# Kernel optimization log

Measured on AMD Instinct MI355X. Metric: run time of the kernel, lower is better.

## Reference

```python
import jax, jax.numpy as jnp
import numpy as np

NUM_CLASSES = 8
UP = 3


def _espcn_params(key):
    k1, k2, k3 = jax.random.split(key, 3)
    # conv1: 5x5, 1->64 ; conv2: 3x3, 64->32 ; conv3: 3x3, 32->UP^2
    w1 = jax.random.normal(k1, (64, 1, 5, 5), jnp.float32) * 0.05
    b1 = jnp.zeros((64,), jnp.float32)
    w2 = jax.random.normal(k2, (32, 64, 3, 3), jnp.float32) * 0.05
    b2 = jnp.zeros((32,), jnp.float32)
    w3 = jax.random.normal(k3, (UP * UP, 32, 3, 3), jnp.float32) * 0.05
    b3 = jnp.zeros((UP * UP,), jnp.float32)
    return (w1, b1, w2, b2, w3, b3)


def setup_inputs() -> dict:
    key = jax.random.key(0)
    kx, kc, kp = jax.random.split(key, 3)
    x = jax.random.uniform(kx, (32, 1, 128, 128), jnp.float32)
    class_indices = jax.random.randint(kc, (32,), 0, NUM_CLASSES, jnp.int32)
    # Stack per-expert params along leading expert axis
    keys = jax.random.split(kp, NUM_CLASSES)
    per = [_espcn_params(k) for k in keys]
    stacked = [jnp.stack([p[i] for p in per], axis=0) for i in range(6)]
    w1, b1, w2, b2, w3, b3 = stacked
    return {"x": x, "class_indices": class_indices,
            "w1": w1, "b1": b1, "w2": w2, "b2": b2, "w3": w3, "b3": b3}


def _conv(x, w, b, pad):
    y = jax.lax.conv_general_dilated(
        x, w, window_strides=(1, 1), padding=[(pad, pad), (pad, pad)],
        dimension_numbers=("NCHW", "OIHW", "NCHW"))
    return y + b[None, :, None, None]


def _pixel_shuffle(x, r):
    b, c, h, w = x.shape
    oc = c // (r * r)
    x = x.reshape(b, oc, r, r, h, w)
    x = x.transpose(0, 1, 4, 2, 5, 3)  # b, oc, h, r, w, r
    return x.reshape(b, oc, h * r, w * r)


def _espcn(x, w1, b1, w2, b2, w3, b3):
    h = jnp.tanh(_conv(x, w1, b1, 2))
    h = jnp.tanh(_conv(h, w2, b2, 1))
    h = _conv(h, w3, b3, 1)
    return _pixel_shuffle(h, UP)


def reference(x, class_indices, w1, b1, w2, b2, w3, b3):
    # Run every expert on the full batch (faithful to original dense dispatch),
    # then mask-and-sum via one-hot routing weights.
    one_hot = jax.nn.one_hot(class_indices, NUM_CLASSES, dtype=x.dtype)  # [B, E]

    def run_expert(params):
        ew1, eb1, ew2, eb2, ew3, eb3 = params
        return _espcn(x, ew1, eb1, ew2, eb2, ew3, eb3)  # [B, C, H*r, W*r]

    outs = jax.vmap(run_expert)((w1, b1, w2, b2, w3, b3))  # [E, B, C, H', W']
    weights = one_hot.T[:, :, None, None, None]  # [E, B, 1, 1, 1]
    return jnp.sum(outs * weights, axis=0)
```

## Files before the change

kernel.cpp:

```cpp
#include <hip/hip_runtime.h>

#define NE 8
#define HW 128
#define OUT_HW 384
#define C1 64
#define C2 32
#define C3 9

typedef __attribute__((ext_vector_type(4))) float f32x4;
typedef __attribute__((ext_vector_type(8))) short bf16x8s;
typedef __attribute__((ext_vector_type(2))) unsigned u32x2;

__device__ __align__(16) unsigned short g_w1b[NE * C1 * 32];
__device__ __align__(16) unsigned short g_w2b[NE * 9 * C2 * C1];
__device__ __align__(16) unsigned short g_w3b[NE * 9 * 16 * 32];

__device__ __forceinline__ unsigned short f2bf(float f) {
    unsigned u = __builtin_bit_cast(unsigned, f);
    u += 0x7fffu + ((u >> 16) & 1u);
    return (unsigned short)(u >> 16);
}

__device__ __forceinline__ unsigned cvt_pk_bf16(float lo, float hi) {
    unsigned r;
    asm("v_cvt_pk_bf16_f32 %0, %1, %2" : "=v"(r) : "v"(lo), "v"(hi));
    return r;
}

__global__ void repack_weights_kernel(const float* __restrict__ w1,
                                      const float* __restrict__ w2,
                                      const float* __restrict__ w3) {
    int i = blockIdx.x * 256 + threadIdx.x;
    const int n2 = NE * C2 * C1 * 9;
    const int n1 = NE * C1 * 32;
    const int n3 = NE * 9 * 16 * 32;
    if (i < n2) {
        int e = i / (C2 * C1 * 9);
        int r = i - e * (C2 * C1 * 9);
        int oc = r / (C1 * 9); r -= oc * (C1 * 9);
        int ic = r / 9;
        int koff = r - ic * 9;
        g_w2b[((e * 9 + koff) * C2 + oc) * C1 + ic] = f2bf(w2[i]);
    } else if (i < n2 + n1) {
        int j = i - n2;
        int tap = j & 31;
        int eoc = j >> 5;
        float v = (tap < 25) ? w1[eoc * 25 + tap] : 0.f;
        g_w1b[j] = f2bf(v);
    } else if (i < n2 + n1 + n3) {
        int j = i - n2 - n1;
        int e = j / (9 * 16 * 32);
        int r = j - e * (9 * 16 * 32);
        int koff = r / 512; r -= koff * 512;
        int oc = r / 32;
        int ic = r - oc * 32;
        float v = 0.f;
        if (oc < C3) v = w3[((e * C3 + oc) * 32 + ic) * 9 + koff];
        g_w3b[((e * 9 + koff) * 16 + oc) * 32 + ic] = f2bf(v);
    }
}

__device__ __forceinline__ float fast_tanh(float x) {
    float u = __builtin_amdgcn_exp2f(x * 2.88539008f);
    return 1.0f - 2.0f * __builtin_amdgcn_rcpf(1.0f + u);
}

__launch_bounds__(512, 4)
__global__ void espcn_fused_kernel(const float* __restrict__ x,
                                   const int* __restrict__ ci,
                                   const float* __restrict__ b1,
                                   const float* __restrict__ b2,
                                   const float* __restrict__ b3,
                                   float* __restrict__ out) {
    __shared__ __align__(16) char ldsp[79200];
    float (*xs)[25]   = (float(*)[25])ldsp;
    char* imc         = ldsp + 2400;
    char* h2b         = ldsp + 2400;
    char* h1s         = ldsp + 28000;
    float (*outT)[52] = (float(*)[52])(ldsp + 28000);

    const int tx = blockIdx.x, ty = blockIdx.y, b = blockIdx.z;
    const int R0 = ty * 16, C0 = tx * 16;
    const bool interior = (tx >= 1) && (tx <= 6) && (ty >= 1) && (ty <= 6);
    int e = ci[b];
    e = __builtin_amdgcn_readfirstlane(e);
    const int t = threadIdx.x;
    const int lane = t & 63, wave = t >> 6;
    const int g = lane >> 4, r16 = lane & 15;

    #pragma unroll
    for (int it = 0; it < 2; ++it) {
        int idx = it * 512 + t;
        if (idx < 576) {
            int ii = idx / 24, jj = idx - ii * 24;
            int gy = R0 - 4 + ii, gx = C0 - 4 + jj;
            float v = 0.f;
            if (interior || ((unsigned)gy < (unsigned)HW && (unsigned)gx < (unsigned)HW))
                v = x[(b * HW + gy) * HW + gx];
            xs[ii][jj] = v;
        }
    }
    __syncthreads();

    {
        const int w = t & 15, pr = t >> 4;
        int t0 = 2 * w;     if (t0 > 24) t0 = 24;
        int t1 = 2 * w + 1; if (t1 > 24) t1 = 24;
        const int dy0 = t0 / 5, dx0 = t0 - 5 * (t0 / 5);
        const int dy1 = t1 / 5, dx1 = t1 - 5 * (t1 / 5);
        const bool v0 = (2 * w) < 25, v1 = (2 * w + 1) < 25;
        const int swz = (w * 4) ^ ((pr & 3) << 4);
        #pragma unroll
        for (int it = 0; it < 13; ++it) {
            int p = it * 32 + pr;
            if (p < 400) {
                int i = p / 20, j = p - i * 20;
                float f0 = v0 ? xs[i + dy0][j + dx0] : 0.f;
                float f1 = v1 ? xs[i + dy1][j + dx1] : 0.f;
                *(unsigned*)(imc + p * 64 + swz) = cvt_pk_bf16(f0, f1);
            }
        }
    }
    __syncthreads();

    {
        const unsigned short* w1e = g_w1b + e * C1 * 32;
        const int octile = wave & 3, hi = wave >> 2;
        bf16x8s W = *(const bf16x8s*)(w1e + (octile * 16 + r16) * 32 + g * 8);
        f32x4 bias4 = *(const f32x4*)(b1 + e * C1 + octile * 16 + g * 4);
        const int imcb = r16 * 64 + ((g * 16) ^ ((r16 & 3) << 4));
        const int h1b = (r16 << 7) + ((octile * 32 + g * 8) ^ ((r16 & 7) << 4));
        #pragma unroll
        for (int k = 0; k < 13; ++k) {
            int pt = hi + 2 * k;
            if (pt < 25) {
                bf16x8s I = *(const bf16x8s*)(imc + pt * 1024 + imcb);
                f32x4 acc = {0.f, 0.f, 0.f, 0.f};
                acc = __builtin_amdgcn_mfma_f32_16x16x32_bf16(W, I, acc, 0, 0, 0);
                float s0 = fast_tanh(acc[0] + bias4[0]);
                float s1 = fast_tanh(acc[1] + bias4[1]);
                float s2 = fast_tanh(acc[2] + bias4[2]);
                float s3 = fast_tanh(acc[3] + bias4[3]);
                if (!interior) {
                    int p = pt * 16 + r16;
                    int i = p / 20, j = p - i * 20;
                    int gy = R0 - 2 + i, gx = C0 - 2 + j;
                    bool in = ((unsigned)gy < (unsigned)HW) && ((unsigned)gx < (unsigned)HW);
                    if (!in) { s0 = 0.f; s1 = 0.f; s2 = 0.f; s3 = 0.f; }
                }
                u32x2 hv = { cvt_pk_bf16(s0, s1), cvt_pk_bf16(s2, s3) };
                *(u32x2*)(h1s + h1b + pt * 2048) = hv;
            }
        }
    }
    __syncthreads();

    {
        const unsigned short* w2e = g_w2b + e * 9 * C2 * C1;
        const bool has2 = (wave + 16) < 21;
        const int pt0 = wave, pt1 = wave + 8, pt2 = has2 ? wave + 16 : wave;
        int ab[3];
        {
            int pts[3] = {pt0, pt1, pt2};
            #pragma unroll
            for (int s3 = 0; s3 < 3; ++s3) {
                int px = pts[s3] * 16 + r16; if (px > 323) px = 323;
                int r = px / 18, c = px - r * 18;
                ab[s3] = r * 20 + c;
            }
        }
        int rb[3][9];
        #pragma unroll
        for (int s3 = 0; s3 < 3; ++s3)
            #pragma unroll
            for (int k = 0; k < 9; ++k) {
                int ap = ab[s3] + (k / 3) * 20 + (k % 3);
                rb[s3][k] = (ap << 7) | ((ap & 7) << 4);
            }
        f32x4 a00 = {0.f,0.f,0.f,0.f}, a01 = {0.f,0.f,0.f,0.f};
        f32x4 a10 = {0.f,0.f,0.f,0.f}, a11 = {0.f,0.f,0.f,0.f};
        f32x4 a20 = {0.f,0.f,0.f,0.f}, a21 = {0.f,0.f,0.f,0.f};
        const int laneB = r16 * C1 + g * 8;
        const int icb = g * 16;
        #pragma unroll
        for (int s = 0; s < 18; ++s) {
            const int koff = s >> 1;
            const int ic = (s & 1) * 64 + icb;
            const unsigned short* wp = w2e + koff * (C2 * C1) + (s & 1) * 32;
            bf16x8s B0 = *(const bf16x8s*)(wp + laneB);
            bf16x8s B1 = *(const bf16x8s*)(wp + laneB + 16 * C1);
            bf16x8s A0 = *(const bf16x8s*)(h1s + (rb[0][koff] ^ ic));
            bf16x8s A1 = *(const bf16x8s*)(h1s + (rb[1][koff] ^ ic));
            a00 = __builtin_amdgcn_mfma_f32_16x16x32_bf16(B0, A0, a00, 0, 0, 0);
            a01 = __builtin_amdgcn_mfma_f32_16x16x32_bf16(B1, A0, a01, 0, 0, 0);
            a10 = __builtin_amdgcn_mfma_f32_16x16x32_bf16(B0, A1, a10, 0, 0, 0);
            a11 = __builtin_amdgcn_mfma_f32_16x16x32_bf16(B1, A1, a11, 0, 0, 0);
            if (has2) {
                bf16x8s A2 = *(const bf16x8s*)(h1s + (rb[2][koff] ^ ic));
                a20 = __builtin_amdgcn_mfma_f32_16x16x32_bf16(B0, A2, a20, 0, 0, 0);
                a21 = __builtin_amdgcn_mfma_f32_16x16x32_bf16(B1, A2, a21, 0, 0, 0);
            }
        }
        const float* b2e = b2 + e * C2;
        f32x4 bias0 = *(const f32x4*)(b2e + g * 4);
        f32x4 bias1 = *(const f32x4*)(b2e + 16 + g * 4);
        const int wb0 = (g * 8) ^ ((r16 & 3) << 4);
        const int wb1 = (32 + g * 8) ^ ((r16 & 3) << 4);
        #pragma unroll
        for (int s3 = 0; s3 < 3; ++s3) {
            int pt = (s3 == 0) ? pt0 : (s3 == 1) ? pt1 : pt2;
            f32x4 aa0 = (s3 == 0) ? a00 : (s3 == 1) ? a10 : a20;
            f32x4 aa1 = (s3 == 0) ? a01 : (s3 == 1) ? a11 : a21;
            int px = pt * 16 + r16;
            bool wvalid = (px < 324) && (s3 != 2 || has2);
            if (wvalid) {
                float u0 = fast_tanh(aa0[0] + bias0[0]);
                float u1 = fast_tanh(aa0[1] + bias0[1]);
                float u2 = fast_tanh(aa0[2] + bias0[2]);
                float u3 = fast_tanh(aa0[3] + bias0[3]);
                float v0 = fast_tanh(aa1[0] + bias1[0]);
                float v1 = fast_tanh(aa1[1] + bias1[1]);
                float v2 = fast_tanh(aa1[2] + bias1[2]);
                float v3 = fast_tanh(aa1[3] + bias1[3]);
                if (!interior) {
                    int y = px / 18, xx = px - y * 18;
                    int gy = R0 - 1 + y, gx = C0 - 1 + xx;
                    bool in = ((unsigned)gy < (unsigned)HW) && ((unsigned)gx < (unsigned)HW);
                    if (!in) {
                        u0 = u1 = u2 = u3 = 0.f;
                        v0 = v1 = v2 = v3 = 0.f;
                    }
                }
                u32x2 h0 = { cvt_pk_bf16(u0, u1), cvt_pk_bf16(u2, u3) };
                u32x2 h1v = { cvt_pk_bf16(v0, v1), cvt_pk_bf16(v2, v3) };
                *(u32x2*)(h2b + (px << 6) + wb0) = h0;
                *(u32x2*)(h2b + (px << 6) + wb1) = h1v;
            }
        }
    }
    __syncthreads();

    {
        const unsigned short* w3e = g_w3b + e * 9 * 16 * 32;
        const int px0 = (wave * 2) * 16 + r16, px1 = (wave * 2 + 1) * 16 + r16;
        const int pb0 = (px0 >> 4) * 18 + (px0 & 15);
        const int pb1 = (px1 >> 4) * 18 + (px1 & 15);
        f32x4 acc0 = {0.f,0.f,0.f,0.f}, acc1 = {0.f,0.f,0.f,0.f};
        #pragma unroll
        for (int s = 0; s < 9; ++s) {
            int d = (s / 3) * 18 + (s % 3);
            int p0 = pb0 + d, p1 = pb1 + d;
            bf16x8s A0 = *(const bf16x8s*)(h2b + ((p0 << 6) | ((g * 16) ^ ((p0 & 3) << 4))));
            bf16x8s A1 = *(const bf16x8s*)(h2b + ((p1 << 6) | ((g * 16) ^ ((p1 & 3) << 4))));
            bf16x8s B = *(const bf16x8s*)(w3e + (s * 16 + r16) * 32 + g * 8);
            acc0 = __builtin_amdgcn_mfma_f32_16x16x32_bf16(A0, B, acc0, 0, 0, 0);
            acc1 = __builtin_amdgcn_mfma_f32_16x16x32_bf16(A1, B, acc1, 0, 0, 0);
        }
        if (r16 < C3) {
            float bias = b3[e * C3 + r16];
            const int ocr = r16 / 3, occ = r16 % 3;
            #pragma unroll
            for (int m = 0; m < 2; ++m) {
                f32x4 a = m ? acc1 : acc0;
                #pragma unroll
                for (int q = 0; q < 4; ++q) {
                    int pxd = (wave * 2 + m) * 16 + g * 4 + q;
                    int oy = pxd >> 4, ox = pxd & 15;
                    outT[oy * 3 + ocr][ox * 3 + occ] = a[q] + bias;
                }
            }
        }
    }
    __syncthreads();

    #pragma unroll
    for (int it = 0; it < 2; ++it) {
        int idx = it * 512 + t;
        if (idx < 576) {
            int row = idx / 12, c4 = idx - row * 12;
            f32x4 v = *(const f32x4*)&outT[row][c4 * 4];
            *(f32x4*)&out[(b * OUT_HW + 48 * ty + row) * OUT_HW + 48 * tx + c4 * 4] = v;
        }
    }
}

extern "C" void kernel_launch(void* const* d_in, const int* in_sizes, int n_in,
                              void* d_out, int out_size, void* d_ws, size_t ws_size,
                              hipStream_t stream) {
    const float* x  = (const float*)d_in[0];
    const int*   ci = (const int*)  d_in[1];
    const float* w1 = (const float*)d_in[2];
    const float* b1 = (const float*)d_in[3];
    const float* w2 = (const float*)d_in[4];
    const float* b2 = (const float*)d_in[5];
    const float* w3 = (const float*)d_in[6];
    const float* b3 = (const float*)d_in[7];
    float* out = (float*)d_out;

    {
        const int total = NE * C2 * C1 * 9 + NE * C1 * 32 + NE * 9 * 16 * 32;
        repack_weights_kernel<<<(total + 255) / 256, 256, 0, stream>>>(w1, w2, w3);
    }
    {
        dim3 grid(HW / 16, HW / 16, 32);
        espcn_fused_kernel<<<grid, 512, 0, stream>>>(x, ci, b1, b2, b3, out);
    }
}
```

Measured before the change: 164.9 us.

## Split conv1/conv2 into two channel halves to shrink LDS footprint

Conv1 output channels are now produced in two halves of 32, and each half is consumed by conv2 before the next half is written. This halves the h1 shared-memory buffer, and the LDS regions are rearranged (xs moved to overlap h1s), cutting shared memory per block from about 79KB to 51KB. Launch bounds are raised to target more resident blocks per CU. The cost is extra barriers per half, including a new sync before outT overwrites the shared buffer, and possible register pressure from the higher occupancy target.

```diff
diff --git a/kernel.cpp b/kernel.cpp
--- a/kernel.cpp
+++ b/kernel.cpp
@@ -65,19 +65,19 @@
     return 1.0f - 2.0f * __builtin_amdgcn_rcpf(1.0f + u);
 }
 
-__launch_bounds__(512, 4)
+__launch_bounds__(512, 6)
 __global__ void espcn_fused_kernel(const float* __restrict__ x,
                                    const int* __restrict__ ci,
                                    const float* __restrict__ b1,
                                    const float* __restrict__ b2,
                                    const float* __restrict__ b3,
                                    float* __restrict__ out) {
-    __shared__ __align__(16) char ldsp[79200];
-    float (*xs)[25]   = (float(*)[25])ldsp;
-    char* imc         = ldsp + 2400;
-    char* h2b         = ldsp + 2400;
-    char* h1s         = ldsp + 28000;
-    float (*outT)[52] = (float(*)[52])(ldsp + 28000);
+    __shared__ __align__(16) char ldsp[51200];
+    char* imc         = ldsp;
+    char* h2b         = ldsp;
+    char* h1s         = ldsp + 25600;
+    float (*xs)[24]   = (float(*)[24])(ldsp + 25600);
+    float (*outT)[52] = (float(*)[52])(ldsp + 25600);
 
     const int tx = blockIdx.x, ty = blockIdx.y, b = blockIdx.z;
     const int R0 = ty * 16, C0 = tx * 16;
@@ -123,84 +123,88 @@
     }
     __syncthreads();
 
-    {
-        const unsigned short* w1e = g_w1b + e * C1 * 32;
-        const int octile = wave & 3, hi = wave >> 2;
-        bf16x8s W = *(const bf16x8s*)(w1e + (octile * 16 + r16) * 32 + g * 8);
-        f32x4 bias4 = *(const f32x4*)(b1 + e * C1 + octile * 16 + g * 4);
-        const int imcb = r16 * 64 + ((g * 16) ^ ((r16 & 3) << 4));
-        const int h1b = (r16 << 7) + ((octile * 32 + g * 8) ^ ((r16 & 7) << 4));
+    const unsigned short* w2e = g_w2b + e * 9 * C2 * C1;
+    const bool has2 = (wave + 16) < 21;
+    const int pt0 = wave, pt1 = wave + 8, pt2 = has2 ? wave + 16 : wave;
+    int rb[3][9];
+    {
+        int pts[3] = {pt0, pt1, pt2};
         #pragma unroll
-        for (int k = 0; k < 13; ++k) {
-            int pt = hi + 2 * k;
-            if (pt < 25) {
-                bf16x8s I = *(const bf16x8s*)(imc + pt * 1024 + imcb);
-                f32x4 acc = {0.f, 0.f, 0.f, 0.f};
-                acc = __builtin_amdgcn_mfma_f32_16x16x32_bf16(W, I, acc, 0, 0, 0);
-                float s0 = fast_tanh(acc[0] + bias4[0]);
-                float s1 = fast_tanh(acc[1] + bias4[1]);
-                float s2 = fast_tanh(acc[2] + bias4[2]);
-                float s3 = fast_tanh(acc[3] + bias4[3]);
-                if (!interior) {
-                    int p = pt * 16 + r16;
-                    int i = p / 20, j = p - i * 20;
-                    int gy = R0 - 2 + i, gx = C0 - 2 + j;
-                    bool in = ((unsigned)gy < (unsigned)HW) && ((unsigned)gx < (unsigned)HW);
-                    if (!in) { s0 = 0.f; s1 = 0.f; s2 = 0.f; s3 = 0.f; }
-                }
-                u32x2 hv = { cvt_pk_bf16(s0, s1), cvt_pk_bf16(s2, s3) };
-                *(u32x2*)(h1s + h1b + pt * 2048) = hv;
-            }
-        }
-    }
-    __syncthreads();
-
-    {
-        const unsigned short* w2e = g_w2b + e * 9 * C2 * C1;
-        const bool has2 = (wave + 16) < 21;
-        const int pt0 = wave, pt1 = wave + 8, pt2 = has2 ? wave + 16 : wave;
-        int ab[3];
-        {
-            int pts[3] = {pt0, pt1, pt2};
-            #pragma unroll
-            for (int s3 = 0; s3 < 3; ++s3) {
-                int px = pts[s3] * 16 + r16; if (px > 323) px = 323;
-                int r = px / 18, c = px - r * 18;
-                ab[s3] = r * 20 + c;
-            }
-        }
-        int rb[3][9];
-        #pragma unroll
-        for (int s3 = 0; s3 < 3; ++s3)
+        for (int s3 = 0; s3 < 3; ++s3) {
+            int px = pts[s3] * 16 + r16; if (px > 323) px = 323;
+            int r = px / 18, c = px - r * 18;
+            int ab = r * 20 + c;
             #pragma unroll
             for (int k = 0; k < 9; ++k) {
-                int ap = ab[s3] + (k / 3) * 20 + (k % 3);
-                rb[s3][k] = (ap << 7) | ((ap & 7) << 4);
-            }
-        f32x4 a00 = {0.f,0.f,0.f,0.f}, a01 = {0.f,0.f,0.f,0.f};
-        f32x4 a10 = {0.f,0.f,0.f,0.f}, a11 = {0.f,0.f,0.f,0.f};
-        f32x4 a20 = {0.f,0.f,0.f,0.f}, a21 = {0.f,0.f,0.f,0.f};
-        const int laneB = r16 * C1 + g * 8;
-        const int icb = g * 16;
-        #pragma unroll
-        for (int s = 0; s < 18; ++s) {
-            const int koff = s >> 1;
-            const int ic = (s & 1) * 64 + icb;
-            const unsigned short* wp = w2e + koff * (C2 * C1) + (s & 1) * 32;
-            bf16x8s B0 = *(const bf16x8s*)(wp + laneB);
-            bf16x8s B1 = *(const bf16x8s*)(wp + laneB + 16 * C1);
-            bf16x8s A0 = *(const bf16x8s*)(h1s + (rb[0][koff] ^ ic));
-            bf16x8s A1 = *(const bf16x8s*)(h1s + (rb[1][koff] ^ ic));
-            a00 = __builtin_amdgcn_mfma_f32_16x16x32_bf16(B0, A0, a00, 0, 0, 0);
-            a01 = __builtin_amdgcn_mfma_f32_16x16x32_bf16(B1, A0, a01, 0, 0, 0);
-            a10 = __builtin_amdgcn_mfma_f32_16x16x32_bf16(B0, A1, a10, 0, 0, 0);
-            a11 = __builtin_amdgcn_mfma_f32_16x16x32_bf16(B1, A1, a11, 0, 0, 0);
-            if (has2) {
-                bf16x8s A2 = *(const bf16x8s*)(h1s + (rb[2][koff] ^ ic));
-                a20 = __builtin_amdgcn_mfma_f32_16x16x32_bf16(B0, A2, a20, 0, 0, 0);
-                a21 = __builtin_amdgcn_mfma_f32_16x16x32_bf16(B1, A2, a21, 0, 0, 0);
-            }
-        }
+                int ap = ab + (k / 3) * 20 + (k % 3);
+                rb[s3][k] = (ap << 6) | ((ap & 3) << 4);
+            }
+        }
+    }
+    f32x4 a00 = {0.f,0.f,0.f,0.f}, a01 = {0.f,0.f,0.f,0.f};
+    f32x4 a10 = {0.f,0.f,0.f,0.f}, a11 = {0.f,0.f,0.f,0.f};
+    f32x4 a20 = {0.f,0.f,0.f,0.f}, a21 = {0.f,0.f,0.f,0.f};
+
+    #pragma unroll
+    for (int half = 0; half < 2; ++half) {
+        {
+            const unsigned short* w1e = g_w1b + e * C1 * 32;
+            const int octile = wave & 1, ptg = wave >> 1;
+            const int ocg = half * 32 + octile * 16;
+            bf16x8s W = *(const bf16x8s*)(w1e + (ocg + r16) * 32 + g * 8);
+            f32x4 bias4 = *(const f32x4*)(b1 + e * C1 + ocg + g * 4);
+            const int imcb = r16 * 64 + ((g * 16) ^ ((r16 & 3) << 4));
+            const int h1b = (r16 << 6) + ((octile * 32 + g * 8) ^ ((r16 & 3) << 4));
+            #pragma unroll
+            for (int k = 0; k < 7; ++k) {
+                int pt = ptg + 4 * k;
+                if (pt < 25) {
+                    bf16x8s I = *(const bf16x8s*)(imc + pt * 1024 + imcb);
+                    f32x4 acc = {0.f, 0.f, 0.f, 0.f};
+                    acc = __builtin_amdgcn_mfma_f32_16x16x32_bf16(W, I, acc, 0, 0, 0);
+                    float s0 = fast_tanh(acc[0] + bias4[0]);
+                    float s1 = fast_tanh(acc[1] + bias4[1]);
+                    float s2 = fast_tanh(acc[2] + bias4[2]);
+                    float s3 = fast_tanh(acc[3] + bias4[3]);
+                    if (!interior) {
+                        int p = pt * 16 + r16;
+                        int i = p / 20, j = p - i * 20;
+                        int gy = R0 - 2 + i, gx = C0 - 2 + j;
+                        bool in = ((unsigned)gy < (unsigned)HW) && ((unsigned)gx < (unsigned)HW);
+                        if (!in) { s0 = 0.f; s1 = 0.f; s2 = 0.f; s3 = 0.f; }
+                    }
+                    u32x2 hv = { cvt_pk_bf16(s0, s1), cvt_pk_bf16(s2, s3) };
+                    *(u32x2*)(h1s + h1b + pt * 1024) = hv;
+                }
+            }
+        }
+        __syncthreads();
+
+        {
+            const int icb = g * 16;
+            const int wB = r16 * C1 + half * 32 + g * 8;
+            #pragma unroll
+            for (int koff = 0; koff < 9; ++koff) {
+                const unsigned short* wp = w2e + koff * (C2 * C1);
+                bf16x8s B0 = *(const bf16x8s*)(wp + wB);
+                bf16x8s B1 = *(const bf16x8s*)(wp + wB + 16 * C1);
+                bf16x8s A0 = *(const bf16x8s*)(h1s + (rb[0][koff] ^ icb));
+                bf16x8s A1 = *(const bf16x8s*)(h1s + (rb[1][koff] ^ icb));
+                a00 = __builtin_amdgcn_mfma_f32_16x16x32_bf16(B0, A0, a00, 0, 0, 0);
+                a01 = __builtin_amdgcn_mfma_f32_16x16x32_bf16(B1, A0, a01, 0, 0, 0);
+                a10 = __builtin_amdgcn_mfma_f32_16x16x32_bf16(B0, A1, a10, 0, 0, 0);
+                a11 = __builtin_amdgcn_mfma_f32_16x16x32_bf16(B1, A1, a11, 0, 0, 0);
+                if (has2) {
+                    bf16x8s A2 = *(const bf16x8s*)(h1s + (rb[2][koff] ^ icb));
+                    a20 = __builtin_amdgcn_mfma_f32_16x16x32_bf16(B0, A2, a20, 0, 0, 0);
+                    a21 = __builtin_amdgcn_mfma_f32_16x16x32_bf16(B1, A2, a21, 0, 0, 0);
+                }
+            }
+        }
+        __syncthreads();
+    }
+
+    {
         const float* b2e = b2 + e * C2;
         f32x4 bias0 = *(const f32x4*)(b2e + g * 4);
         f32x4 bias1 = *(const f32x4*)(b2e + 16 + g * 4);
@@ -256,6 +260,7 @@
             acc0 = __builtin_amdgcn_mfma_f32_16x16x32_bf16(A0, B, acc0, 0, 0, 0);
             acc1 = __builtin_amdgcn_mfma_f32_16x16x32_bf16(A1, B, acc1, 0, 0, 0);
         }
+        __syncthreads();
         if (r16 < C3) {
             float bias = b3[e * C3 + r16];
             const int ocr = r16 / 3, occ = r16 % 3;
```

Measured after the change: 189.7 us. 15.1% more time.
